# Optimization experiments

Measured on AMD Instinct MI355X. Metric: run time of the kernel, lower is better.

Reference implementation:

```python
import jax, jax.numpy as jnp
import numpy as np

H = 16
D_MODEL = 1024
D_K = D_MODEL // H
NEG = -1e9


def setup_inputs() -> dict:
    key = jax.random.key(0)
    ks = jax.random.split(key, 12)
    B, S = 2, 2048
    inp = {
        "query": jax.random.normal(ks[0], (B, S, D_MODEL), jnp.float32),
        "key": jax.random.normal(ks[1], (B, S, D_MODEL), jnp.float32),
        "value": jax.random.normal(ks[2], (B, S, D_MODEL), jnp.float32),
        "mask": jnp.ones((B, 1, S), jnp.int32),
    }
    s = 1.0 / np.sqrt(D_MODEL)
    for i, nm in enumerate(["Wq", "Wk", "Wv", "Wo"]):
        inp[nm] = jax.random.normal(ks[3 + i], (D_MODEL, D_MODEL), jnp.float32) * s
        inp["b" + nm[1]] = jax.random.normal(ks[7 + i], (D_MODEL,), jnp.float32) * s
    return inp


def _split_heads(x):
    B, S, _ = x.shape
    return x.reshape(B, S, H, D_K).transpose(0, 2, 1, 3)  # [B,H,S,Dk]


def reference(query, key, value, mask, Wq, bq, Wk, bk, Wv, bv, Wo, bo):
    q = _split_heads(query @ Wq + bq)
    k = _split_heads(key @ Wk + bk)
    v = _split_heads(value @ Wv + bv)
    scores = jnp.einsum("bhqd,bhkd->bhqk", q, k) / jnp.sqrt(jnp.float32(D_K))
    # mask [B,1,Sk] -> broadcast as [B,1,1,Sk]
    scores = jnp.where(mask[:, None, :, :] == 0, NEG, scores)
    attn = jax.nn.softmax(scores, axis=-1)  # dropout is identity in eval mode
    out = jnp.einsum("bhqk,bhkd->bhqd", attn, v)
    B, _, Sq, _ = out.shape
    out = out.transpose(0, 2, 1, 3).reshape(B, Sq, H * D_K)
    return out @ Wo + bo
```

## Files before the change

kernel.cpp:

```cpp
#include <hip/hip_runtime.h>
#include <hip/hip_bf16.h>

typedef __attribute__((ext_vector_type(8))) short short8;
typedef __attribute__((ext_vector_type(4))) float float4v;
typedef __hip_bfloat16 bf16;

#define MFMA16(a, b, c) __builtin_amdgcn_mfma_f32_16x16x32_bf16((a), (b), (c), 0, 0, 0)

static __device__ __forceinline__ short8 load8(const bf16* p) {
    return *reinterpret_cast<const short8*>(p);
}
static __device__ __forceinline__ unsigned short bfu(float x) {
    union { bf16 b; unsigned short u; } c; c.b = __float2bfloat16(x); return c.u;
}
static __device__ __forceinline__ unsigned pack2(float lo, float hi) {
    return ((unsigned)bfu(hi) << 16) | bfu(lo);
}
static __device__ __forceinline__ short bf_bits(float x) {
    union { bf16 b; short u; } c; c.b = __float2bfloat16(x); return c.u;
}
static __device__ __forceinline__ short8 cvt8(float4 a, float4 b) {
    short8 r;
    r[0] = bf_bits(a.x); r[1] = bf_bits(a.y); r[2] = bf_bits(a.z); r[3] = bf_bits(a.w);
    r[4] = bf_bits(b.x); r[5] = bf_bits(b.y); r[6] = bf_bits(b.z); r[7] = bf_bits(b.w);
    return r;
}

typedef const __attribute__((address_space(1))) unsigned int* gp1;
typedef __attribute__((address_space(3))) unsigned int* lp3;
static __device__ __forceinline__ void async16(const void* g, void* l) {
    __builtin_amdgcn_global_load_lds((gp1)g, (lp3)l, 16, 0, 0);
}

__global__ __launch_bounds__(256) void transpose_qkv(
    const float* __restrict__ Wq, const float* __restrict__ Wk,
    const float* __restrict__ Wv, bf16* __restrict__ out_base)
{
    __shared__ bf16 tile[64][65];
    const float* in = (blockIdx.z == 0) ? Wq : (blockIdx.z == 1) ? Wk : Wv;
    bf16* out = out_base + (size_t)blockIdx.z * 1048576;
    int tx = threadIdx.x, ty = threadIdx.y;
    int bx = blockIdx.x * 64, by = blockIdx.y * 64;
    for (int i = ty; i < 64; i += 4)
        tile[i][tx] = __float2bfloat16(in[(size_t)(by + i) * 1024 + bx + tx]);
    __syncthreads();
    for (int i = ty; i < 64; i += 4)
        out[(size_t)(bx + i) * 1024 + by + tx] = tile[tx][i];
}

__global__ __launch_bounds__(256) void transpose_one(
    const float* __restrict__ in, bf16* __restrict__ out)
{
    __shared__ bf16 tile[64][65];
    int tx = threadIdx.x, ty = threadIdx.y;
    int bx = blockIdx.x * 64, by = blockIdx.y * 64;
    for (int i = ty; i < 64; i += 4)
        tile[i][tx] = __float2bfloat16(in[(size_t)(by + i) * 1024 + bx + tx]);
    __syncthreads();
    for (int i = ty; i < 64; i += 4)
        out[(size_t)(bx + i) * 1024 + by + tx] = tile[tx][i];
}

__global__ __launch_bounds__(256, 3) void qkv_gemm(
    const float* __restrict__ Xq, const float* __restrict__ Xk,
    const float* __restrict__ Xv, const bf16* __restrict__ Wt_all,
    const float* __restrict__ bq, const float* __restrict__ bk,
    const float* __restrict__ bv,
    bf16* __restrict__ outq, bf16* __restrict__ outk, bf16* __restrict__ outv)
{
    __shared__ float As[2][128 * 32];
    __shared__ bf16  Bs[2][128 * 32];

    int wg = blockIdx.x;
    int xcd = wg & 7;
    int jj = wg >> 3;
    int grp = xcd * 12 + (jj >> 3);
    int z = grp >> 5;
    int m_blk = grp & 31;
    int n_blk = jj & 7;

    const float* X    = (z == 0) ? Xq : (z == 1) ? Xk : Xv;
    const float* bias = (z == 0) ? bq : (z == 1) ? bk : bv;
    const bf16*  Wt   = Wt_all + (size_t)z * 1048576;
    bf16*        out  = (z == 0) ? outq : (z == 1) ? outk : outv;
    bool vmode = (z == 2);

    int tid = threadIdx.x;
    int w = tid >> 6, lane = tid & 63, l16 = lane & 15, quad = lane >> 4;
    int m_base = m_blk * 128, n_base = n_blk * 128;

    int ra = lane >> 3;
    int sa = (lane & 7) ^ (ra & 7);
    int rb = lane >> 2;
    int sb = (lane & 3) ^ (rb & 3);
    const float* Asrc = X  + (size_t)(m_base + w * 8 + ra) * 1024 + sa * 4;
    const bf16*  Bsrc = Wt + (size_t)(n_base + w * 16 + rb) * 1024 + sb * 8;

    int wm = (w & 1) * 64, wn = (w >> 1) * 64;

    float4v zero = {0.f, 0.f, 0.f, 0.f};
    float4v acc[4][4];
    #pragma unroll
    for (int mi = 0; mi < 4; ++mi)
        #pragma unroll
        for (int nj = 0; nj < 4; ++nj) acc[mi][nj] = zero;

    #pragma unroll
    for (int p = 0; p < 4; ++p)
        async16(Asrc + (size_t)p * 32 * 1024, (char*)As[0] + w * 1024 + p * 4096);
    #pragma unroll
    for (int p = 0; p < 2; ++p)
        async16(Bsrc + (size_t)p * 64 * 1024, (char*)Bs[0] + w * 1024 + p * 4096);
    __syncthreads();

    for (int it = 0; it < 32; ++it) {
        int cur = it & 1, nxt = cur ^ 1;
        int kn = ((it + 1) & 31) * 32;

        #pragma unroll
        for (int p = 0; p < 4; ++p)
            async16(Asrc + (size_t)p * 32 * 1024 + kn,
                    (char*)As[nxt] + w * 1024 + p * 4096);
        #pragma unroll
        for (int p = 0; p < 2; ++p)
            async16(Bsrc + (size_t)p * 64 * 1024 + kn,
                    (char*)Bs[nxt] + w * 1024 + p * 4096);

        short8 af[4], bf[4];
        #pragma unroll
        for (int mi = 0; mi < 4; ++mi) {
            const float* rp = As[cur] + (wm + mi * 16 + l16) * 32;
            float4 f0 = *(const float4*)(rp + (((quad * 2)     ^ (l16 & 7)) << 2));
            float4 f1 = *(const float4*)(rp + (((quad * 2 + 1) ^ (l16 & 7)) << 2));
            af[mi] = cvt8(f0, f1);
        }
        #pragma unroll
        for (int nj = 0; nj < 4; ++nj) {
            const bf16* rp = Bs[cur] + (wn + nj * 16 + l16) * 32;
            bf[nj] = load8(rp + ((quad ^ (l16 & 3)) << 3));
        }
        #pragma unroll
        for (int mi = 0; mi < 4; ++mi)
            #pragma unroll
            for (int nj = 0; nj < 4; ++nj)
                acc[mi][nj] = MFMA16(af[mi], bf[nj], acc[mi][nj]);
        __syncthreads();
    }

    float bsv[4];
    #pragma unroll
    for (int nj = 0; nj < 4; ++nj)
        bsv[nj] = bias[n_base + wn + nj * 16 + l16];

    #pragma unroll
    for (int mi = 0; mi < 4; ++mi) {
        #pragma unroll
        for (int nj = 0; nj < 4; ++nj) {
            int n = n_base + wn + nj * 16 + l16;
            int h = n >> 6, dk = n & 63;
            int m0 = m_base + wm + mi * 16 + quad * 4;
            int b = m0 >> 11, s0 = m0 & 2047;
            if (vmode) {
                float v0 = acc[mi][nj][0] + bsv[nj];
                float v1 = acc[mi][nj][1] + bsv[nj];
                float v2 = acc[mi][nj][2] + bsv[nj];
                float v3 = acc[mi][nj][3] + bsv[nj];
                uint2 pv; pv.x = pack2(v0, v1); pv.y = pack2(v2, v3);
                size_t idx = ((size_t)(b * 16 + h) * 64 + dk) * 2048 + s0;
                *reinterpret_cast<uint2*>(out + idx) = pv;
            } else {
                #pragma unroll
                for (int r = 0; r < 4; ++r) {
                    size_t idx = (((size_t)(b * 16 + h) * 2048 + s0 + r) * 64 + dk);
                    out[idx] = __float2bfloat16(acc[mi][nj][r] + bsv[nj]);
                }
            }
        }
    }
}

__global__ __launch_bounds__(256, 2) void out_gemm(
    const bf16* __restrict__ A, const bf16* __restrict__ Wt,
    const float* __restrict__ bias, float* __restrict__ out)
{
    __shared__ bf16 As[2][128 * 32];
    __shared__ bf16 Bs[2][64 * 32];

    int wg = blockIdx.x;
    int xcd = wg & 7;
    int jj = wg >> 3;
    int m_blk = xcd * 4 + (jj >> 4);
    int n_blk = jj & 15;

    int tid = threadIdx.x;
    int w = tid >> 6, lane = tid & 63, l16 = lane & 15, quad = lane >> 4;
    int m_base = m_blk * 128, n_base = n_blk * 64;

    int rr = lane >> 2;
    int ss = (lane & 3) ^ (rr & 3);
    const bf16* Asrc = A  + (size_t)(m_base + w * 16 + rr) * 1024 + ss * 8;
    const bf16* Bsrc = Wt + (size_t)(n_base + w * 16 + rr) * 1024 + ss * 8;

    int wm = (w & 1) * 64, wn = (w >> 1) * 32;

    float4v zero = {0.f, 0.f, 0.f, 0.f};
    float4v acc[4][2];
    #pragma unroll
    for (int mi = 0; mi < 4; ++mi)
        #pragma unroll
        for (int nj = 0; nj < 2; ++nj) acc[mi][nj] = zero;

    #pragma unroll
    for (int p = 0; p < 2; ++p)
        async16(Asrc + (size_t)p * 64 * 1024, (char*)As[0] + w * 1024 + p * 4096);
    async16(Bsrc, (char*)Bs[0] + w * 1024);
    __syncthreads();

    for (int it = 0; it < 32; ++it) {
        int cur = it & 1, nxt = cur ^ 1;
        int kn = ((it + 1) & 31) * 32;

        #pragma unroll
        for (int p = 0; p < 2; ++p)
            async16(Asrc + (size_t)p * 64 * 1024 + kn,
                    (char*)As[nxt] + w * 1024 + p * 4096);
        async16(Bsrc + kn, (char*)Bs[nxt] + w * 1024);

        short8 af[4], bf[2];
        #pragma unroll
        for (int mi = 0; mi < 4; ++mi) {
            const bf16* rp = As[cur] + (wm + mi * 16 + l16) * 32;
            af[mi] = load8(rp + ((quad ^ (l16 & 3)) << 3));
        }
        #pragma unroll
        for (int nj = 0; nj < 2; ++nj) {
            const bf16* rp = Bs[cur] + (wn + nj * 16 + l16) * 32;
            bf[nj] = load8(rp + ((quad ^ (l16 & 3)) << 3));
        }
        #pragma unroll
        for (int mi = 0; mi < 4; ++mi)
            #pragma unroll
            for (int nj = 0; nj < 2; ++nj)
                acc[mi][nj] = MFMA16(af[mi], bf[nj], acc[mi][nj]);
        __syncthreads();
    }

    float bsv[2];
    #pragma unroll
    for (int nj = 0; nj < 2; ++nj)
        bsv[nj] = bias[n_base + wn + nj * 16 + l16];

    #pragma unroll
    for (int mi = 0; mi < 4; ++mi)
        #pragma unroll
        for (int nj = 0; nj < 2; ++nj) {
            int n = n_base + wn + nj * 16 + l16;
            int m0 = m_base + wm + mi * 16 + quad * 4;
            #pragma unroll
            for (int r = 0; r < 4; ++r)
                out[(size_t)(m0 + r) * 1024 + n] = acc[mi][nj][r] + bsv[nj];
        }
}

__global__ __launch_bounds__(256, 4) void attn_fused(
    const bf16* __restrict__ Qm, const bf16* __restrict__ Km,
    const bf16* __restrict__ Vt, const int* __restrict__ mask,
    bf16* __restrict__ Oout)
{
    __shared__ __align__(16) bf16 Kc[64 * 64];
    __shared__ __align__(16) bf16 Vc[64 * 64];
    __shared__ __align__(16) bf16 P[4][32 * 72];
    __shared__ unsigned long long maskb[32];

    int tid = threadIdx.x;
    int w = tid >> 6, lane = tid & 63, l16 = lane & 15, quad = lane >> 4;
    int wg = blockIdx.x;
    int xcd = wg & 7;
    int jj = wg >> 3;
    int bh = xcd * 4 + (jj >> 4);
    int qg = jj & 15;
    int b = bh >> 4, h = bh & 15;
    int tile0 = (qg * 4 + w) * 2;

    const int* mb = mask + b * 2048;
    #pragma unroll
    for (int i = 0; i < 8; ++i) {
        unsigned long long bal = __ballot(mb[w * 512 + i * 64 + lane] != 0);
        if (lane == 0) maskb[w * 8 + i] = bal;
    }

    short8 bQ[2][2];
    #pragma unroll
    for (int qi = 0; qi < 2; ++qi) {
        const bf16* Qb = Qm + ((size_t)bh * 2048 + (size_t)(tile0 + qi) * 16) * 64;
        bQ[qi][0] = load8(Qb + l16 * 64 + quad * 8);
        bQ[qi][1] = load8(Qb + l16 * 64 + 32 + quad * 8);
    }

    int r8 = lane >> 3;
    int sl = (lane & 7) ^ (r8 & 7);
    const bf16* Ksrc = Km + (size_t)bh * 2048 * 64 + (size_t)(w * 8 + r8) * 64 + sl * 8;
    const bf16* Vsrc = Vt + (size_t)bh * 64 * 2048 + (size_t)(w * 8 + r8) * 2048 + sl * 8;
    char* Kdst = (char*)Kc + w * 1024;
    char* Vdst = (char*)Vc + w * 1024;

    bf16* Pw = &P[w][0];
    int sw = l16 & 7;

    float4v zero = {0.f, 0.f, 0.f, 0.f};
    float4v Oacc[2][4];
    #pragma unroll
    for (int qi = 0; qi < 2; ++qi)
        #pragma unroll
        for (int g = 0; g < 4; ++g) Oacc[qi][g] = zero;
    float lsum[2] = {0.f, 0.f};
    const float C = 0.18033688f;

    for (int it = 0; it < 32; ++it) {
        int kt = it * 64;
        async16(Ksrc + (size_t)kt * 64, Kdst);
        async16(Ksrc + (size_t)(kt + 32) * 64, Kdst + 4096);
        async16(Vsrc + kt, Vdst);
        async16(Vsrc + (size_t)32 * 2048 + kt, Vdst + 4096);
        __syncthreads();

        unsigned long long m64 = maskb[it];
        bool full = (m64 == ~0ull);

        float4v S[2][4];
        #pragma unroll
        for (int kj = 0; kj < 4; ++kj) {
            const bf16* kr = Kc + (kj * 16 + l16) * 64;
            short8 a0 = load8(kr + (((0 + quad) ^ sw) << 3));
            short8 a1 = load8(kr + (((4 + quad) ^ sw) << 3));
            #pragma unroll
            for (int qi = 0; qi < 2; ++qi) {
                float4v s = zero;
                s = MFMA16(a0, bQ[qi][0], s);
                s = MFMA16(a1, bQ[qi][1], s);
                S[qi][kj] = s;
            }
        }

        #pragma unroll
        for (int kj = 0; kj < 4; ++kj) {
            unsigned m4 = (unsigned)(m64 >> (kj * 16 + quad * 4)) & 0xFu;
            #pragma unroll
            for (int qi = 0; qi < 2; ++qi) {
                float p[4];
                #pragma unroll
                for (int r = 0; r < 4; ++r)
                    p[r] = __builtin_amdgcn_exp2f(S[qi][kj][r] * C);
                if (!full) {
                    #pragma unroll
                    for (int r = 0; r < 4; ++r)
                        p[r] = ((m4 >> r) & 1u) ? p[r] : 0.f;
                }
                lsum[qi] += (p[0] + p[1]) + (p[2] + p[3]);
                uint2 pw; pw.x = pack2(p[0], p[1]); pw.y = pack2(p[2], p[3]);
                *reinterpret_cast<uint2*>(
                    &Pw[(qi * 16 + l16) * 72 + kj * 16 + quad * 4]) = pw;
            }
        }

        short8 ap[2][2];
        #pragma unroll
        for (int qi = 0; qi < 2; ++qi) {
            ap[qi][0] = load8(&Pw[(qi * 16 + l16) * 72 + quad * 8]);
            ap[qi][1] = load8(&Pw[(qi * 16 + l16) * 72 + 32 + quad * 8]);
        }
        #pragma unroll
        for (int g = 0; g < 4; ++g) {
            const bf16* vr = Vc + (g * 16 + l16) * 64;
            short8 v0 = load8(vr + (((0 + quad) ^ sw) << 3));
            short8 v1 = load8(vr + (((4 + quad) ^ sw) << 3));
            #pragma unroll
            for (int qi = 0; qi < 2; ++qi) {
                Oacc[qi][g] = MFMA16(ap[qi][0], v0, Oacc[qi][g]);
                Oacc[qi][g] = MFMA16(ap[qi][1], v1, Oacc[qi][g]);
            }
        }
        __syncthreads();
    }

    #pragma unroll
    for (int qi = 0; qi < 2; ++qi) {
        float ls = lsum[qi];
        ls += __shfl_xor(ls, 16, 64);
        ls += __shfl_xor(ls, 32, 64);
        #pragma unroll
        for (int r = 0; r < 4; ++r) {
            float linv = 1.f / __shfl(ls, quad * 4 + r, 64);
            int srow = (tile0 + qi) * 16 + quad * 4 + r;
            size_t base = ((size_t)b * 2048 + srow) * 1024 + h * 64;
            #pragma unroll
            for (int g = 0; g < 4; ++g)
                Oout[base + g * 16 + l16] = __float2bfloat16(Oacc[qi][g][r] * linv);
        }
    }
}

extern "C" void kernel_launch(void* const* d_in, const int* in_sizes, int n_in,
                              void* d_out, int out_size, void* d_ws, size_t ws_size,
                              hipStream_t stream) {
    const float* query = (const float*)d_in[0];
    const float* key   = (const float*)d_in[1];
    const float* value = (const float*)d_in[2];
    const int*   mask  = (const int*)d_in[3];
    const float* Wq = (const float*)d_in[4];
    const float* bq = (const float*)d_in[5];
    const float* Wk = (const float*)d_in[6];
    const float* bk = (const float*)d_in[7];
    const float* Wv = (const float*)d_in[8];
    const float* bv = (const float*)d_in[9];
    const float* Wo = (const float*)d_in[10];
    const float* bo = (const float*)d_in[11];

    char* ws = (char*)d_ws;
    const size_t MB = 1024 * 1024;
    bf16* vb     = (bf16*)ws;
    bf16* Wt_all = (bf16*)(ws + 8 * MB);
    bf16* aout   = (bf16*)(ws + 8 * MB);
    bf16* WtO    = (bf16*)ws;
    bf16* qb     = (bf16*)d_out;
    bf16* kb     = (bf16*)((char*)d_out + 8 * MB);
    float* out   = (float*)d_out;

    transpose_qkv<<<dim3(16, 16, 3), dim3(64, 4), 0, stream>>>(Wq, Wk, Wv, Wt_all);

    qkv_gemm<<<dim3(768), 256, 0, stream>>>(
        query, key, value, Wt_all, bq, bk, bv, qb, kb, vb);

    attn_fused<<<dim3(512), 256, 0, stream>>>(qb, kb, vb, mask, aout);

    transpose_one<<<dim3(16, 16), dim3(64, 4), 0, stream>>>(Wo, WtO);

    out_gemm<<<dim3(512), 256, 0, stream>>>(aout, WtO, bo, out);
}
```

Before: 274.2 us.

## Replace double-buffered K=32 tiles with single-buffered K=64 tiles in GEMMs and attention

```diff
diff --git a/kernel.cpp b/kernel.cpp
--- a/kernel.cpp
+++ b/kernel.cpp
@@ -68,8 +68,8 @@
     const float* __restrict__ bv,
     bf16* __restrict__ outq, bf16* __restrict__ outk, bf16* __restrict__ outv)
 {
-    __shared__ float As[2][128 * 32];
-    __shared__ bf16  Bs[2][128 * 32];
+    __shared__ float As[128 * 64];
+    __shared__ bf16  Bs[128 * 64];
 
     int wg = blockIdx.x;
     int xcd = wg & 7;
@@ -89,14 +89,14 @@
     int w = tid >> 6, lane = tid & 63, l16 = lane & 15, quad = lane >> 4;
     int m_base = m_blk * 128, n_base = n_blk * 128;
 
-    int ra = lane >> 3;
-    int sa = (lane & 7) ^ (ra & 7);
-    int rb = lane >> 2;
-    int sb = (lane & 3) ^ (rb & 3);
-    const float* Asrc = X  + (size_t)(m_base + w * 8 + ra) * 1024 + sa * 4;
-    const bf16*  Bsrc = Wt + (size_t)(n_base + w * 16 + rb) * 1024 + sb * 8;
+    int r4 = lane >> 4, s16 = lane & 15;
+    int r8 = lane >> 3, s8 = lane & 7;
+    const float* Asrc0 = X + (size_t)(m_base + w * 32 + r4) * 1024 + ((s16 ^ r4) << 2);
+    const float* Asrc1 = X + (size_t)(m_base + w * 32 + r4) * 1024 + ((s16 ^ (4 + r4)) << 2);
+    const bf16*  Bsrc  = Wt + (size_t)(n_base + w * 32 + r8) * 1024 + ((s8 ^ r8) << 3);
 
     int wm = (w & 1) * 64, wn = (w >> 1) * 64;
+    int sw = l16 & 7;
 
     float4v zero = {0.f, 0.f, 0.f, 0.f};
     float4v acc[4][4];
@@ -105,45 +105,39 @@
         #pragma unroll
         for (int nj = 0; nj < 4; ++nj) acc[mi][nj] = zero;
 
-    #pragma unroll
-    for (int p = 0; p < 4; ++p)
-        async16(Asrc + (size_t)p * 32 * 1024, (char*)As[0] + w * 1024 + p * 4096);
-    #pragma unroll
-    for (int p = 0; p < 2; ++p)
-        async16(Bsrc + (size_t)p * 64 * 1024, (char*)Bs[0] + w * 1024 + p * 4096);
-    __syncthreads();
-
-    for (int it = 0; it < 32; ++it) {
-        int cur = it & 1, nxt = cur ^ 1;
-        int kn = ((it + 1) & 31) * 32;
-
+    for (int it = 0; it < 16; ++it) {
+        int kt = it * 64;
+        #pragma unroll
+        for (int p = 0; p < 8; ++p) {
+            const float* s = ((p & 1) ? Asrc1 : Asrc0) + (size_t)p * 4096 + kt;
+            async16(s, (char*)As + (w * 32 + p * 4) * 256);
+        }
         #pragma unroll
         for (int p = 0; p < 4; ++p)
-            async16(Asrc + (size_t)p * 32 * 1024 + kn,
-                    (char*)As[nxt] + w * 1024 + p * 4096);
-        #pragma unroll
-        for (int p = 0; p < 2; ++p)
-            async16(Bsrc + (size_t)p * 64 * 1024 + kn,
-                    (char*)Bs[nxt] + w * 1024 + p * 4096);
-
-        short8 af[4], bf[4];
-        #pragma unroll
-        for (int mi = 0; mi < 4; ++mi) {
-            const float* rp = As[cur] + (wm + mi * 16 + l16) * 32;
-            float4 f0 = *(const float4*)(rp + (((quad * 2)     ^ (l16 & 7)) << 2));
-            float4 f1 = *(const float4*)(rp + (((quad * 2 + 1) ^ (l16 & 7)) << 2));
-            af[mi] = cvt8(f0, f1);
-        }
-        #pragma unroll
-        for (int nj = 0; nj < 4; ++nj) {
-            const bf16* rp = Bs[cur] + (wn + nj * 16 + l16) * 32;
-            bf[nj] = load8(rp + ((quad ^ (l16 & 3)) << 3));
-        }
-        #pragma unroll
-        for (int mi = 0; mi < 4; ++mi)
-            #pragma unroll
-            for (int nj = 0; nj < 4; ++nj)
-                acc[mi][nj] = MFMA16(af[mi], bf[nj], acc[mi][nj]);
+            async16(Bsrc + (size_t)p * 8192 + kt, (char*)Bs + (w * 32 + p * 8) * 128);
+        __syncthreads();
+
+        #pragma unroll
+        for (int kk = 0; kk < 2; ++kk) {
+            short8 af[4], bfr[4];
+            #pragma unroll
+            for (int mi = 0; mi < 4; ++mi) {
+                const float* rp = As + (wm + mi * 16 + l16) * 64;
+                float4 f0 = *(const float4*)(rp + (((kk * 8 + quad * 2)     ^ sw) << 2));
+                float4 f1 = *(const float4*)(rp + (((kk * 8 + quad * 2 + 1) ^ sw) << 2));
+                af[mi] = cvt8(f0, f1);
+            }
+            #pragma unroll
+            for (int nj = 0; nj < 4; ++nj) {
+                const bf16* rp = Bs + (wn + nj * 16 + l16) * 64;
+                bfr[nj] = load8(rp + (((kk * 4 + quad) ^ sw) << 3));
+            }
+            #pragma unroll
+            for (int mi = 0; mi < 4; ++mi)
+                #pragma unroll
+                for (int nj = 0; nj < 4; ++nj)
+                    acc[mi][nj] = MFMA16(af[mi], bfr[nj], acc[mi][nj]);
+        }
         __syncthreads();
     }
 
@@ -183,8 +177,8 @@
     const bf16* __restrict__ A, const bf16* __restrict__ Wt,
     const float* __restrict__ bias, float* __restrict__ out)
 {
-    __shared__ bf16 As[2][128 * 32];
-    __shared__ bf16 Bs[2][64 * 32];
+    __shared__ bf16 As[128 * 64];
+    __shared__ bf16 Bs[64 * 64];
 
     int wg = blockIdx.x;
     int xcd = wg & 7;
@@ -196,12 +190,12 @@
     int w = tid >> 6, lane = tid & 63, l16 = lane & 15, quad = lane >> 4;
     int m_base = m_blk * 128, n_base = n_blk * 64;
 
-    int rr = lane >> 2;
-    int ss = (lane & 3) ^ (rr & 3);
-    const bf16* Asrc = A  + (size_t)(m_base + w * 16 + rr) * 1024 + ss * 8;
-    const bf16* Bsrc = Wt + (size_t)(n_base + w * 16 + rr) * 1024 + ss * 8;
+    int r8 = lane >> 3, s8 = lane & 7;
+    const bf16* Asrc = A  + (size_t)(m_base + w * 32 + r8) * 1024 + ((s8 ^ r8) << 3);
+    const bf16* Bsrc = Wt + (size_t)(n_base + w * 16 + r8) * 1024 + ((s8 ^ r8) << 3);
 
     int wm = (w & 1) * 64, wn = (w >> 1) * 32;
+    int sw = l16 & 7;
 
     float4v zero = {0.f, 0.f, 0.f, 0.f};
     float4v acc[4][2];
@@ -210,38 +204,35 @@
         #pragma unroll
         for (int nj = 0; nj < 2; ++nj) acc[mi][nj] = zero;
 
-    #pragma unroll
-    for (int p = 0; p < 2; ++p)
-        async16(Asrc + (size_t)p * 64 * 1024, (char*)As[0] + w * 1024 + p * 4096);
-    async16(Bsrc, (char*)Bs[0] + w * 1024);
-    __syncthreads();
-
-    for (int it = 0; it < 32; ++it) {
-        int cur = it & 1, nxt = cur ^ 1;
-        int kn = ((it + 1) & 31) * 32;
-
+    for (int it = 0; it < 16; ++it) {
+        int kt = it * 64;
+        #pragma unroll
+        for (int p = 0; p < 4; ++p)
+            async16(Asrc + (size_t)p * 8192 + kt, (char*)As + (w * 32 + p * 8) * 128);
         #pragma unroll
         for (int p = 0; p < 2; ++p)
-            async16(Asrc + (size_t)p * 64 * 1024 + kn,
-                    (char*)As[nxt] + w * 1024 + p * 4096);
-        async16(Bsrc + kn, (char*)Bs[nxt] + w * 1024);
-
-        short8 af[4], bf[2];
-        #pragma unroll
-        for (int mi = 0; mi < 4; ++mi) {
-            const bf16* rp = As[cur] + (wm + mi * 16 + l16) * 32;
-            af[mi] = load8(rp + ((quad ^ (l16 & 3)) << 3));
-        }
-        #pragma unroll
-        for (int nj = 0; nj < 2; ++nj) {
-            const bf16* rp = Bs[cur] + (wn + nj * 16 + l16) * 32;
-            bf[nj] = load8(rp + ((quad ^ (l16 & 3)) << 3));
-        }
-        #pragma unroll
-        for (int mi = 0; mi < 4; ++mi)
-            #pragma unroll
-            for (int nj = 0; nj < 2; ++nj)
-                acc[mi][nj] = MFMA16(af[mi], bf[nj], acc[mi][nj]);
+            async16(Bsrc + (size_t)p * 8192 + kt, (char*)Bs + (w * 16 + p * 8) * 128);
+        __syncthreads();
+
+        #pragma unroll
+        for (int kk = 0; kk < 2; ++kk) {
+            short8 af[4], bfr[2];
+            #pragma unroll
+            for (int mi = 0; mi < 4; ++mi) {
+                const bf16* rp = As + (wm + mi * 16 + l16) * 64;
+                af[mi] = load8(rp + (((kk * 4 + quad) ^ sw) << 3));
+            }
+            #pragma unroll
+            for (int nj = 0; nj < 2; ++nj) {
+                const bf16* rp = Bs + (wn + nj * 16 + l16) * 64;
+                bfr[nj] = load8(rp + (((kk * 4 + quad) ^ sw) << 3));
+            }
+            #pragma unroll
+            for (int mi = 0; mi < 4; ++mi)
+                #pragma unroll
+                for (int nj = 0; nj < 2; ++nj)
+                    acc[mi][nj] = MFMA16(af[mi], bfr[nj], acc[mi][nj]);
+        }
         __syncthreads();
     }
 
@@ -262,13 +253,13 @@
         }
 }
 
-__global__ __launch_bounds__(256, 4) void attn_fused(
+__global__ __launch_bounds__(256, 3) void attn_fused(
     const bf16* __restrict__ Qm, const bf16* __restrict__ Km,
     const bf16* __restrict__ Vt, const int* __restrict__ mask,
     bf16* __restrict__ Oout)
 {
-    __shared__ __align__(16) bf16 Kc[64 * 64];
-    __shared__ __align__(16) bf16 Vc[64 * 64];
+    __shared__ __align__(16) bf16 Kc[128 * 64];
+    __shared__ __align__(16) bf16 Vc[64 * 128];
     __shared__ __align__(16) bf16 P[4][32 * 72];
     __shared__ unsigned long long maskb[32];
 
@@ -297,12 +288,11 @@
         bQ[qi][1] = load8(Qb + l16 * 64 + 32 + quad * 8);
     }
 
-    int r8 = lane >> 3;
-    int sl = (lane & 7) ^ (r8 & 7);
-    const bf16* Ksrc = Km + (size_t)bh * 2048 * 64 + (size_t)(w * 8 + r8) * 64 + sl * 8;
-    const bf16* Vsrc = Vt + (size_t)bh * 64 * 2048 + (size_t)(w * 8 + r8) * 2048 + sl * 8;
-    char* Kdst = (char*)Kc + w * 1024;
-    char* Vdst = (char*)Vc + w * 1024;
+    int r8 = lane >> 3, s8 = lane & 7;
+    int r4 = lane >> 4, s16 = lane & 15;
+    const bf16* Ksrc  = Km + (size_t)bh * 131072 + (size_t)(w * 32 + r8) * 64 + ((s8 ^ r8) << 3);
+    const bf16* Vsrc0 = Vt + (size_t)bh * 131072 + (size_t)(w * 16 + r4) * 2048 + ((s16 ^ r4) << 3);
+    const bf16* Vsrc1 = Vt + (size_t)bh * 131072 + (size_t)(w * 16 + r4) * 2048 + ((s16 ^ (4 + r4)) << 3);
 
     bf16* Pw = &P[w][0];
     int sw = l16 & 7;
@@ -316,68 +306,75 @@
     float lsum[2] = {0.f, 0.f};
     const float C = 0.18033688f;
 
-    for (int it = 0; it < 32; ++it) {
-        int kt = it * 64;
-        async16(Ksrc + (size_t)kt * 64, Kdst);
-        async16(Ksrc + (size_t)(kt + 32) * 64, Kdst + 4096);
-        async16(Vsrc + kt, Vdst);
-        async16(Vsrc + (size_t)32 * 2048 + kt, Vdst + 4096);
-        __syncthreads();
-
-        unsigned long long m64 = maskb[it];
-        bool full = (m64 == ~0ull);
-
-        float4v S[2][4];
-        #pragma unroll
-        for (int kj = 0; kj < 4; ++kj) {
-            const bf16* kr = Kc + (kj * 16 + l16) * 64;
-            short8 a0 = load8(kr + (((0 + quad) ^ sw) << 3));
-            short8 a1 = load8(kr + (((4 + quad) ^ sw) << 3));
-            #pragma unroll
-            for (int qi = 0; qi < 2; ++qi) {
-                float4v s = zero;
-                s = MFMA16(a0, bQ[qi][0], s);
-                s = MFMA16(a1, bQ[qi][1], s);
-                S[qi][kj] = s;
-            }
-        }
-
-        #pragma unroll
-        for (int kj = 0; kj < 4; ++kj) {
-            unsigned m4 = (unsigned)(m64 >> (kj * 16 + quad * 4)) & 0xFu;
-            #pragma unroll
-            for (int qi = 0; qi < 2; ++qi) {
-                float p[4];
-                #pragma unroll
-                for (int r = 0; r < 4; ++r)
-                    p[r] = __builtin_amdgcn_exp2f(S[qi][kj][r] * C);
-                if (!full) {
+    for (int it = 0; it < 16; ++it) {
+        int kt = it * 128;
+        #pragma unroll
+        for (int p = 0; p < 4; ++p)
+            async16(Ksrc + (size_t)(kt + p * 8) * 64, (char*)Kc + (w * 32 + p * 8) * 128);
+        #pragma unroll
+        for (int p = 0; p < 4; ++p) {
+            const bf16* s = ((p & 1) ? Vsrc1 : Vsrc0) + (size_t)p * 8192 + kt;
+            async16(s, (char*)Vc + (w * 16 + p * 4) * 256);
+        }
+        __syncthreads();
+
+        #pragma unroll
+        for (int hh = 0; hh < 2; ++hh) {
+            unsigned long long m64 = maskb[it * 2 + hh];
+            bool full = (m64 == ~0ull);
+
+            float4v S[2][4];
+            #pragma unroll
+            for (int kj = 0; kj < 4; ++kj) {
+                const bf16* kr = Kc + (hh * 64 + kj * 16 + l16) * 64;
+                short8 a0 = load8(kr + (((0 + quad) ^ sw) << 3));
+                short8 a1 = load8(kr + (((4 + quad) ^ sw) << 3));
+                #pragma unroll
+                for (int qi = 0; qi < 2; ++qi) {
+                    float4v s = zero;
+                    s = MFMA16(a0, bQ[qi][0], s);
+                    s = MFMA16(a1, bQ[qi][1], s);
+                    S[qi][kj] = s;
+                }
+            }
+
+            #pragma unroll
+            for (int kj = 0; kj < 4; ++kj) {
+                unsigned m4 = (unsigned)(m64 >> (kj * 16 + quad * 4)) & 0xFu;
+                #pragma unroll
+                for (int qi = 0; qi < 2; ++qi) {
+                    float p[4];
                     #pragma unroll
                     for (int r = 0; r < 4; ++r)
-                        p[r] = ((m4 >> r) & 1u) ? p[r] : 0.f;
+                        p[r] = __builtin_amdgcn_exp2f(S[qi][kj][r] * C);
+                    if (!full) {
+                        #pragma unroll
+                        for (int r = 0; r < 4; ++r)
+                            p[r] = ((m4 >> r) & 1u) ? p[r] : 0.f;
+                    }
+                    lsum[qi] += (p[0] + p[1]) + (p[2] + p[3]);
+                    uint2 pw; pw.x = pack2(p[0], p[1]); pw.y = pack2(p[2], p[3]);
+                    *reinterpret_cast<uint2*>(
+                        &Pw[(qi * 16 + l16) * 72 + kj * 16 + quad * 4]) = pw;
                 }
-                lsum[qi] += (p[0] + p[1]) + (p[2] + p[3]);
-                uint2 pw; pw.x = pack2(p[0], p[1]); pw.y = pack2(p[2], p[3]);
-                *reinterpret_cast<uint2*>(
-                    &Pw[(qi * 16 + l16) * 72 + kj * 16 + quad * 4]) = pw;
-            }
-        }
-
-        short8 ap[2][2];
-        #pragma unroll
-        for (int qi = 0; qi < 2; ++qi) {
-            ap[qi][0] = load8(&Pw[(qi * 16 + l16) * 72 + quad * 8]);
-            ap[qi][1] = load8(&Pw[(qi * 16 + l16) * 72 + 32 + quad * 8]);
-        }
-        #pragma unroll
-        for (int g = 0; g < 4; ++g) {
-            const bf16* vr = Vc + (g * 16 + l16) * 64;
-            short8 v0 = load8(vr + (((0 + quad) ^ sw) << 3));
-            short8 v1 = load8(vr + (((4 + quad) ^ sw) << 3));
+            }
+
+            short8 ap[2][2];
             #pragma unroll
             for (int qi = 0; qi < 2; ++qi) {
-                Oacc[qi][g] = MFMA16(ap[qi][0], v0, Oacc[qi][g]);
-                Oacc[qi][g] = MFMA16(ap[qi][1], v1, Oacc[qi][g]);
+                ap[qi][0] = load8(&Pw[(qi * 16 + l16) * 72 + quad * 8]);
+                ap[qi][1] = load8(&Pw[(qi * 16 + l16) * 72 + 32 + quad * 8]);
+            }
+            #pragma unroll
+            for (int g = 0; g < 4; ++g) {
+                const bf16* vr = Vc + (g * 16 + l16) * 128;
+                short8 v0 = load8(vr + (((hh * 8 + 0 + quad) ^ sw) << 3));
+                short8 v1 = load8(vr + (((hh * 8 + 4 + quad) ^ sw) << 3));
+                #pragma unroll
+                for (int qi = 0; qi < 2; ++qi) {
+                    Oacc[qi][g] = MFMA16(ap[qi][0], v0, Oacc[qi][g]);
+                    Oacc[qi][g] = MFMA16(ap[qi][1], v1, Oacc[qi][g]);
+                }
             }
         }
         __syncthreads();
```

Result: faster. 251.2 us (-8.4%).
